# Kernel optimization log

Hardware: AMD Instinct MI355X
Metric: run time of the kernel (lower is better)

## Reference

```python
import jax, jax.numpy as jnp
import numpy as np

B, T, V, D, OUT = 32, 100, 10000, 128, 1000
CODE_P = 0.003  # ~30 active codes per visit


def gru_dir(x3, whh, bhh, reverse):
    """x3: [B,T,3F] precomputed input-side gates (W_ih x + b_ih). PyTorch GRU math."""
    F = whh.shape[1]
    h0 = jnp.zeros((x3.shape[0], F), x3.dtype)

    def step(h, xt):
        gh = h @ whh.T + bhh
        xr, xz, xn = jnp.split(xt, 3, -1)
        hr, hz, hn = jnp.split(gh, 3, -1)
        r = jax.nn.sigmoid(xr + hr)
        z = jax.nn.sigmoid(xz + hz)
        n = jnp.tanh(xn + r * hn)
        h_new = (1.0 - z) * n + z * h
        return h_new, h_new

    _, hs = jax.lax.scan(step, h0, jnp.swapaxes(x3, 0, 1), reverse=reverse)
    return jnp.swapaxes(hs, 0, 1)  # [B,T,F]


def setup_inputs() -> dict:
    key = jax.random.key(0)
    ks = jax.random.split(key, 16)
    s = lambda k, *sh: jax.random.normal(k, sh, dtype=jnp.float32) * 0.05
    # multi-hot visits, ~0/1 with density CODE_P; force code 0 present so no all-zero visit
    x = (jax.random.uniform(ks[0], (B, T, V)) < CODE_P).astype(jnp.float32)
    x = x.at[:, :, 0].set(1.0)
    return {
        "batchdata": x,
        "emb": s(ks[1], V, D),
        "wih_f": s(ks[2], 3 * D, D), "whh_f": s(ks[3], 3 * D, D),
        "bih_f": jnp.zeros((3 * D,), jnp.float32), "bhh_f": jnp.zeros((3 * D,), jnp.float32),
        "wih_b": s(ks[4], 3 * D, D), "whh_b": s(ks[5], 3 * D, D),
        "bih_b": jnp.zeros((3 * D,), jnp.float32), "bhh_b": jnp.zeros((3 * D,), jnp.float32),
        "attn_w": s(ks[6], 2 * D, 1), "attn_b": jnp.zeros((1,), jnp.float32),
        "comb_w": s(ks[7], D, 4 * D), "comb_b": jnp.zeros((D,), jnp.float32),
        "fc_w": s(ks[8], OUT, D), "fc_b": jnp.zeros((OUT,), jnp.float32),
    }


def reference(batchdata, emb, wih_f, whh_f, bih_f, bhh_f, wih_b, whh_b, bih_b, bhh_b,
              attn_w, attn_b, comb_w, comb_b, fc_w, fc_b):
    # multihot_to_embedding: sum of embedding rows where visit==1 == multihot @ table
    e = jnp.einsum('btv,vd->btd', batchdata, emb)          # [B,T,D]
    mask = jnp.any(e != 0, axis=2)                          # [B,T]
    # DipoleLayer: bidirectional GRU (hidden=D each dir), dropout in eval mode = identity
    xf = jnp.einsum('btf,gf->btg', e, wih_f) + bih_f
    xb = jnp.einsum('btf,gf->btg', e, wih_b) + bih_b
    hf = gru_dir(xf, whh_f, bhh_f, reverse=False)
    hb = gru_dir(xb, whh_b, bhh_b, reverse=True)
    h = jnp.concatenate([hf, hb], axis=-1)                  # [B,T,2D]
    # location-based attention over timesteps
    scores = (h @ attn_w)[..., 0] + attn_b[0]               # [B,T]
    scores = jnp.where(mask, scores, jnp.float32(-1e9))
    a = jax.nn.softmax(scores, axis=-1)
    c = jnp.einsum('bt,btf->bf', a, h)                      # [B,2D] context
    last = jnp.sum(mask.astype(jnp.int32), axis=-1) - 1     # last valid visit
    h_last = h[jnp.arange(h.shape[0]), last]                # [B,2D]
    feat = jnp.tanh(jnp.concatenate([c, h_last], -1) @ comb_w.T + comb_b)  # [B,D]
    logits = feat @ fc_w.T + fc_b                           # [B,OUT]
    return logits
```

## Files before the change

### kernel.cpp

```cpp
#include <hip/hip_runtime.h>
#include <math.h>

#define BB 32
#define TT 100
#define VV 10000
#define DD 128
#define OUTN 1000
#define G3 384

__global__ __launch_bounds__(256) void k_embed(
    const float* __restrict__ x, const float* __restrict__ emb,
    float* __restrict__ e, int* __restrict__ mask)
{
    const int bt  = blockIdx.x;
    const int tid = threadIdx.x;
    __shared__ int   s_cnt;
    __shared__ int   s_any;
    __shared__ int   s_idx[256];
    __shared__ float s_val[256];
    if (tid == 0) { s_cnt = 0; s_any = 0; }
    __syncthreads();

    const float4* x4 = (const float4*)(x + (size_t)bt * VV);
    for (int i = tid; i < VV / 4; i += 256) {
        float4 v = x4[i];
        if (v.x != 0.f) { int p = atomicAdd(&s_cnt, 1); if (p < 256) { s_idx[p] = 4*i+0; s_val[p] = v.x; } }
        if (v.y != 0.f) { int p = atomicAdd(&s_cnt, 1); if (p < 256) { s_idx[p] = 4*i+1; s_val[p] = v.y; } }
        if (v.z != 0.f) { int p = atomicAdd(&s_cnt, 1); if (p < 256) { s_idx[p] = 4*i+2; s_val[p] = v.z; } }
        if (v.w != 0.f) { int p = atomicAdd(&s_cnt, 1); if (p < 256) { s_idx[p] = 4*i+3; s_val[p] = v.w; } }
    }
    __syncthreads();
    int cnt = s_cnt; if (cnt > 256) cnt = 256;
    if (tid < DD) {
        float acc = 0.f;
        for (int i = 0; i < cnt; ++i)
            acc += s_val[i] * emb[(size_t)s_idx[i] * DD + tid];
        e[(size_t)bt * DD + tid] = acc;
        if (acc != 0.f) s_any = 1;
    }
    __syncthreads();
    if (tid == 0) mask[bt] = s_any;
}

__global__ __launch_bounds__(256) void k_gates(
    const float* __restrict__ e,
    const float* __restrict__ wih_f, const float* __restrict__ bih_f,
    const float* __restrict__ wih_b, const float* __restrict__ bih_b,
    float* __restrict__ x3)
{
    const int r0  = blockIdx.x * 8;
    const int tid = threadIdx.x;
    __shared__ __align__(16) float se[8][DD];
    for (int i = tid; i < 8 * DD; i += 256)
        se[i >> 7][i & 127] = e[(size_t)(r0 + (i >> 7)) * DD + (i & 127)];
    __syncthreads();

    for (int cc = 0; cc < 3; ++cc) {
        const int col = tid + cc * 256;
        const float* wrow;
        float bias;
        if (col < G3) { wrow = wih_f + (size_t)col * DD;        bias = bih_f[col]; }
        else          { wrow = wih_b + (size_t)(col - G3) * DD; bias = bih_b[col - G3]; }
        float acc[8];
        #pragma unroll
        for (int r = 0; r < 8; ++r) acc[r] = 0.f;
        const float4* w4 = (const float4*)wrow;
        for (int k4 = 0; k4 < DD / 4; ++k4) {
            float4 w = w4[k4];
            #pragma unroll
            for (int r = 0; r < 8; ++r) {
                float4 ev = *(const float4*)&se[r][4 * k4];
                acc[r] += ev.x * w.x + ev.y * w.y + ev.z * w.z + ev.w * w.w;
            }
        }
        #pragma unroll
        for (int r = 0; r < 8; ++r)
            x3[(size_t)(r0 + r) * 768 + col] = acc[r] + bias;
    }
}

__device__ __forceinline__ float4 ld_pin_b128(const float4* p)
{
    float4 r;
    asm volatile("global_load_dwordx4 %0, %1, off" : "=v"(r) : "v"(p));
    return r;
}

__global__ __launch_bounds__(512, 2) void k_gru(
    const float* __restrict__ x3,
    const float* __restrict__ whh_f, const float* __restrict__ bhh_f,
    const float* __restrict__ whh_b, const float* __restrict__ bhh_b,
    float* __restrict__ h_all)
{
    const int dir = blockIdx.x & 1;
    const int b   = blockIdx.x >> 1;
    const int tid = threadIdx.x;
    const int g   = tid & 127;
    const int kq  = tid >> 7;
    const int kb  = kq * 32;
    const float* whh = dir ? whh_b : whh_f;
    const float* bhh = dir ? bhh_b : bhh_f;

    const float4* pr4 = (const float4*)(whh + (size_t)(g         ) * DD + kb);
    const float4* pz4 = (const float4*)(whh + (size_t)(DD     + g) * DD + kb);
    const float4* pn4 = (const float4*)(whh + (size_t)(2 * DD + g) * DD + kb);

#define Q8(M) M(0) M(1) M(2) M(3) M(4) M(5) M(6) M(7)
#define DECLW(i) float4 wr##i = ld_pin_b128(pr4 + (i)); \
                 float4 wz##i = ld_pin_b128(pz4 + (i)); \
                 float4 wn##i = ld_pin_b128(pn4 + (i));
    Q8(DECLW)
#undef DECLW
    asm volatile("s_waitcnt vmcnt(0)" ::: "memory");
    __builtin_amdgcn_sched_barrier(0);

    float bhr = 0.f, bhz = 0.f, bhn = 0.f;
    if (tid < DD) { bhr = bhh[g]; bhz = bhh[DD + g]; bhn = bhh[2 * DD + g]; }

    __shared__ __align__(16) float h_lds[DD];
    __shared__ float p_lds[9 * DD];
    float h_reg = 0.f;
    if (tid < DD) h_lds[tid] = 0.f;

    float xr = 0.f, xz = 0.f, xn = 0.f;
    {
        const float* x3p = x3 + (size_t)(b * TT + (dir ? TT - 1 : 0)) * 768 + dir * G3;
        if (tid < DD) { xr = x3p[g]; xz = x3p[DD + g]; xn = x3p[2 * DD + g]; }
    }
    __syncthreads();

    for (int t = 0; t < TT; ++t) {
        const int te = dir ? (TT - 1 - t) : t;

        float nxr = 0.f, nxz = 0.f, nxn = 0.f;
        if (t + 1 < TT) {
            const int tn = dir ? (TT - 2 - t) : (t + 1);
            const float* x3n = x3 + (size_t)(b * TT + tn) * 768 + dir * G3;
            if (tid < DD) { nxr = x3n[g]; nxz = x3n[DD + g]; nxn = x3n[2 * DD + g]; }
        }

        float ar0 = 0.f, ar1 = 0.f, az0 = 0.f, az1 = 0.f, an0 = 0.f, an1 = 0.f;
#define FMA(i) { float4 hv = *(const float4*)&h_lds[kb + 4 * (i)]; \
        (((i)&1) ? ar1 : ar0) += wr##i.x*hv.x + wr##i.y*hv.y + wr##i.z*hv.z + wr##i.w*hv.w; \
        (((i)&1) ? az1 : az0) += wz##i.x*hv.x + wz##i.y*hv.y + wz##i.z*hv.z + wz##i.w*hv.w; \
        (((i)&1) ? an1 : an0) += wn##i.x*hv.x + wn##i.y*hv.y + wn##i.z*hv.z + wn##i.w*hv.w; }
        Q8(FMA)
#undef FMA
        const float pr = ar0 + ar1, pz = az0 + az1, pn = an0 + an1;

        if (kq) {
            const int q = (kq - 1) * 3;
            p_lds[(q + 0) * DD + g] = pr;
            p_lds[(q + 1) * DD + g] = pz;
            p_lds[(q + 2) * DD + g] = pn;
        }
        __syncthreads();

        if (tid < DD) {
            float hr = pr + p_lds[0*DD+g] + p_lds[3*DD+g] + p_lds[6*DD+g] + bhr;
            float hz = pz + p_lds[1*DD+g] + p_lds[4*DD+g] + p_lds[7*DD+g] + bhz;
            float hn = pn + p_lds[2*DD+g] + p_lds[5*DD+g] + p_lds[8*DD+g] + bhn;
            float r  = __builtin_amdgcn_rcpf(1.f + __expf(-(xr + hr)));
            float z  = __builtin_amdgcn_rcpf(1.f + __expf(-(xz + hz)));
            float e2 = __expf(2.f * (xn + r * hn));
            float n  = 1.f - 2.f * __builtin_amdgcn_rcpf(e2 + 1.f);
            float hnew = n + z * (h_reg - n);
            h_reg = hnew;
            h_lds[g] = hnew;
            h_all[(size_t)((dir * BB + b) * TT + te) * DD + g] = hnew;
        }
        __syncthreads();
        xr = nxr; xz = nxz; xn = nxn;
    }
#undef Q8
}

__global__ __launch_bounds__(256) void k_attn(
    const float* __restrict__ h_all, const int* __restrict__ mask,
    const float* __restrict__ attn_w, const float* __restrict__ attn_b,
    const float* __restrict__ comb_w, const float* __restrict__ comb_b,
    float* __restrict__ feat)
{
    const int b   = blockIdx.x;
    const int tid = threadIdx.x;
    __shared__ float s_aw[256];
    __shared__ float s_sc[128];
    __shared__ int   s_m[128];
    __shared__ float s_red[128];
    __shared__ __align__(16) float s_ch[512];

    s_aw[tid] = attn_w[tid];
    int m = 0;
    if (tid < 128) {
        m = (tid < TT) ? mask[b * TT + tid] : 0;
        s_m[tid] = m;
    }
    __syncthreads();
    for (int s = 64; s > 0; s >>= 1) {
        if (tid < s) s_m[tid] += s_m[tid + s];
        __syncthreads();
    }
    const int last = s_m[0] - 1;

    const float* hf = h_all + (size_t)(0 * BB + b) * TT * DD;
    const float* hb = h_all + (size_t)(1 * BB + b) * TT * DD;

    float sc = -1e9f;
    if (tid < TT) {
        float a = attn_b[0];
        const float4* hf4 = (const float4*)(hf + (size_t)tid * DD);
        const float4* hb4 = (const float4*)(hb + (size_t)tid * DD);
        for (int k = 0; k < DD / 4; ++k) {
            float4 v = hf4[k];
            a += v.x * s_aw[4*k] + v.y * s_aw[4*k+1] + v.z * s_aw[4*k+2] + v.w * s_aw[4*k+3];
        }
        for (int k = 0; k < DD / 4; ++k) {
            float4 v = hb4[k];
            a += v.x * s_aw[DD+4*k] + v.y * s_aw[DD+4*k+1] + v.z * s_aw[DD+4*k+2] + v.w * s_aw[DD+4*k+3];
        }
        sc = m ? a : -1e9f;
    }
    if (tid < 128) { s_sc[tid] = sc; s_red[tid] = sc; }
    __syncthreads();
    for (int s = 64; s > 0; s >>= 1) {
        if (tid < s) s_red[tid] = fmaxf(s_red[tid], s_red[tid + s]);
        __syncthreads();
    }
    const float mx = s_red[0];
    __syncthreads();
    float ex = 0.f;
    if (tid < 128) { ex = __expf(s_sc[tid] - mx); s_sc[tid] = ex; s_red[tid] = ex; }
    __syncthreads();
    for (int s = 64; s > 0; s >>= 1) {
        if (tid < s) s_red[tid] += s_red[tid + s];
        __syncthreads();
    }
    const float inv = 1.f / s_red[0];
    __syncthreads();

    {
        const int fl = tid & 127;
        const float* hp = (tid < 128) ? hf : hb;
        float csum = 0.f;
        for (int t = 0; t < TT; ++t)
            csum += s_sc[t] * hp[(size_t)t * DD + fl];
        s_ch[tid]       = csum * inv;
        s_ch[256 + tid] = hp[(size_t)last * DD + fl];
    }
    __syncthreads();

    if (tid < 128) {
        float a = comb_b[tid];
        const float4* cw = (const float4*)(comb_w + (size_t)tid * 512);
        for (int k = 0; k < 128; ++k) {
            float4 w4 = cw[k];
            float4 v4 = *(const float4*)&s_ch[4 * k];
            a += w4.x * v4.x + w4.y * v4.y + w4.z * v4.z + w4.w * v4.w;
        }
        feat[(size_t)b * DD + tid] = tanhf(a);
    }
}

__global__ __launch_bounds__(256) void k_logits(
    const float* __restrict__ feat, const float* __restrict__ fc_w,
    const float* __restrict__ fc_b, float* __restrict__ out)
{
    const int b   = blockIdx.x >> 2;
    const int oc  = blockIdx.x & 3;
    const int tid = threadIdx.x;
    const int o   = oc * 256 + tid;
    __shared__ __align__(16) float s_f[DD];
    if (tid < DD) s_f[tid] = feat[(size_t)b * DD + tid];
    __syncthreads();
    if (o < OUTN) {
        float a = fc_b[o];
        const float4* w4 = (const float4*)(fc_w + (size_t)o * DD);
        for (int k = 0; k < DD / 4; ++k) {
            float4 w = w4[k];
            float4 v = *(const float4*)&s_f[4 * k];
            a += w.x * v.x + w.y * v.y + w.z * v.z + w.w * v.w;
        }
        out[(size_t)b * OUTN + o] = a;
    }
}

extern "C" void kernel_launch(void* const* d_in, const int* in_sizes, int n_in,
                              void* d_out, int out_size, void* d_ws, size_t ws_size,
                              hipStream_t stream)
{
    const float* x      = (const float*)d_in[0];
    const float* emb    = (const float*)d_in[1];
    const float* wih_f  = (const float*)d_in[2];
    const float* whh_f  = (const float*)d_in[3];
    const float* bih_f  = (const float*)d_in[4];
    const float* bhh_f  = (const float*)d_in[5];
    const float* wih_b  = (const float*)d_in[6];
    const float* whh_b  = (const float*)d_in[7];
    const float* bih_b  = (const float*)d_in[8];
    const float* bhh_b  = (const float*)d_in[9];
    const float* attn_w = (const float*)d_in[10];
    const float* attn_b = (const float*)d_in[11];
    const float* comb_w = (const float*)d_in[12];
    const float* comb_b = (const float*)d_in[13];
    const float* fc_w   = (const float*)d_in[14];
    const float* fc_b   = (const float*)d_in[15];
    float* out = (float*)d_out;

    float* ws    = (float*)d_ws;
    float* e     = ws;
    int*   mask  = (int*)(ws + 409600);
    float* x3    = ws + 412800;
    float* h_all = ws + 2870400;
    float* feat  = ws + 3689600;

    k_embed <<<BB * TT,      256, 0, stream>>>(x, emb, e, mask);
    k_gates <<<(BB * TT)/8,  256, 0, stream>>>(e, wih_f, bih_f, wih_b, bih_b, x3);
    k_gru   <<<2 * BB,       512, 0, stream>>>(x3, whh_f, bhh_f, whh_b, bhh_b, h_all);
    k_attn  <<<BB,           256, 0, stream>>>(h_all, mask, attn_w, attn_b, comb_w, comb_b, feat);
    k_logits<<<BB * 4,       256, 0, stream>>>(feat, fc_w, fc_b, out);
}
```

Baseline: 354.5 us.

## Fuse embedding into gate GEMM and logits into attention kernel

The multi-hot embedding gather now happens inside the gate-projection kernel, so each block builds 8 embedding rows in shared memory and never writes or rereads the intermediate e buffer. The gather is unrolled into four independent accumulators. The final FC layer moves into the attention kernel, dropping one launch and the feat round-trip. The GRU launch bound changes from 2 to 1 blocks per SM, which frees registers. The trade-off is that the embed stage drops from 3200 blocks to 400, each scanning 8 rows serially, and the logits stage runs on only 32 blocks.

```diff
diff --git a/kernel.cpp b/kernel.cpp
--- a/kernel.cpp
+++ b/kernel.cpp
@@ -8,53 +8,51 @@
 #define OUTN 1000
 #define G3 384
 
-__global__ __launch_bounds__(256) void k_embed(
+__global__ __launch_bounds__(256) void k_embgate(
     const float* __restrict__ x, const float* __restrict__ emb,
-    float* __restrict__ e, int* __restrict__ mask)
-{
-    const int bt  = blockIdx.x;
+    const float* __restrict__ wih_f, const float* __restrict__ bih_f,
+    const float* __restrict__ wih_b, const float* __restrict__ bih_b,
+    float* __restrict__ x3, int* __restrict__ mask)
+{
+    const int r0  = blockIdx.x * 8;
     const int tid = threadIdx.x;
     __shared__ int   s_cnt;
     __shared__ int   s_any;
     __shared__ int   s_idx[256];
     __shared__ float s_val[256];
-    if (tid == 0) { s_cnt = 0; s_any = 0; }
-    __syncthreads();
-
-    const float4* x4 = (const float4*)(x + (size_t)bt * VV);
-    for (int i = tid; i < VV / 4; i += 256) {
-        float4 v = x4[i];
-        if (v.x != 0.f) { int p = atomicAdd(&s_cnt, 1); if (p < 256) { s_idx[p] = 4*i+0; s_val[p] = v.x; } }
-        if (v.y != 0.f) { int p = atomicAdd(&s_cnt, 1); if (p < 256) { s_idx[p] = 4*i+1; s_val[p] = v.y; } }
-        if (v.z != 0.f) { int p = atomicAdd(&s_cnt, 1); if (p < 256) { s_idx[p] = 4*i+2; s_val[p] = v.z; } }
-        if (v.w != 0.f) { int p = atomicAdd(&s_cnt, 1); if (p < 256) { s_idx[p] = 4*i+3; s_val[p] = v.w; } }
-    }
-    __syncthreads();
-    int cnt = s_cnt; if (cnt > 256) cnt = 256;
-    if (tid < DD) {
-        float acc = 0.f;
-        for (int i = 0; i < cnt; ++i)
-            acc += s_val[i] * emb[(size_t)s_idx[i] * DD + tid];
-        e[(size_t)bt * DD + tid] = acc;
-        if (acc != 0.f) s_any = 1;
-    }
-    __syncthreads();
-    if (tid == 0) mask[bt] = s_any;
-}
-
-__global__ __launch_bounds__(256) void k_gates(
-    const float* __restrict__ e,
-    const float* __restrict__ wih_f, const float* __restrict__ bih_f,
-    const float* __restrict__ wih_b, const float* __restrict__ bih_b,
-    float* __restrict__ x3)
-{
-    const int r0  = blockIdx.x * 8;
-    const int tid = threadIdx.x;
     __shared__ __align__(16) float se[8][DD];
-    for (int i = tid; i < 8 * DD; i += 256)
-        se[i >> 7][i & 127] = e[(size_t)(r0 + (i >> 7)) * DD + (i & 127)];
-    __syncthreads();
-
+
+    for (int r = 0; r < 8; ++r) {
+        if (tid == 0) { s_cnt = 0; s_any = 0; }
+        __syncthreads();
+        const float4* x4 = (const float4*)(x + (size_t)(r0 + r) * VV);
+        for (int i = tid; i < VV / 4; i += 256) {
+            float4 v = x4[i];
+            if (v.x != 0.f) { int p = atomicAdd(&s_cnt, 1); if (p < 256) { s_idx[p] = 4*i+0; s_val[p] = v.x; } }
+            if (v.y != 0.f) { int p = atomicAdd(&s_cnt, 1); if (p < 256) { s_idx[p] = 4*i+1; s_val[p] = v.y; } }
+            if (v.z != 0.f) { int p = atomicAdd(&s_cnt, 1); if (p < 256) { s_idx[p] = 4*i+2; s_val[p] = v.z; } }
+            if (v.w != 0.f) { int p = atomicAdd(&s_cnt, 1); if (p < 256) { s_idx[p] = 4*i+3; s_val[p] = v.w; } }
+        }
+        __syncthreads();
+        int cnt = s_cnt; if (cnt > 256) cnt = 256;
+        if (tid < DD) {
+            float a0 = 0.f, a1 = 0.f, a2 = 0.f, a3 = 0.f;
+            int i = 0;
+            for (; i + 3 < cnt; i += 4) {
+                a0 += s_val[i+0] * emb[(size_t)s_idx[i+0] * DD + tid];
+                a1 += s_val[i+1] * emb[(size_t)s_idx[i+1] * DD + tid];
+                a2 += s_val[i+2] * emb[(size_t)s_idx[i+2] * DD + tid];
+                a3 += s_val[i+3] * emb[(size_t)s_idx[i+3] * DD + tid];
+            }
+            for (; i < cnt; ++i)
+                a0 += s_val[i] * emb[(size_t)s_idx[i] * DD + tid];
+            float acc = (a0 + a1) + (a2 + a3);
+            se[r][tid] = acc;
+            if (acc != 0.f) s_any = 1;
+        }
+        __syncthreads();
+        if (tid == 0) mask[r0 + r] = s_any;
+    }
     for (int cc = 0; cc < 3; ++cc) {
         const int col = tid + cc * 256;
         const float* wrow;
@@ -86,7 +84,7 @@
     return r;
 }
 
-__global__ __launch_bounds__(512, 2) void k_gru(
+__global__ __launch_bounds__(512, 1) void k_gru(
     const float* __restrict__ x3,
     const float* __restrict__ whh_f, const float* __restrict__ bhh_f,
     const float* __restrict__ whh_b, const float* __restrict__ bhh_b,
@@ -175,11 +173,12 @@
 #undef Q8
 }
 
-__global__ __launch_bounds__(256) void k_attn(
+__global__ __launch_bounds__(256) void k_attn_logits(
     const float* __restrict__ h_all, const int* __restrict__ mask,
     const float* __restrict__ attn_w, const float* __restrict__ attn_b,
     const float* __restrict__ comb_w, const float* __restrict__ comb_b,
-    float* __restrict__ feat)
+    const float* __restrict__ fc_w, const float* __restrict__ fc_b,
+    float* __restrict__ out)
 {
     const int b   = blockIdx.x;
     const int tid = threadIdx.x;
@@ -188,6 +187,7 @@
     __shared__ int   s_m[128];
     __shared__ float s_red[128];
     __shared__ __align__(16) float s_ch[512];
+    __shared__ __align__(16) float s_feat[128];
 
     s_aw[tid] = attn_w[tid];
     int m = 0;
@@ -257,30 +257,23 @@
             float4 v4 = *(const float4*)&s_ch[4 * k];
             a += w4.x * v4.x + w4.y * v4.y + w4.z * v4.z + w4.w * v4.w;
         }
-        feat[(size_t)b * DD + tid] = tanhf(a);
-    }
-}
-
-__global__ __launch_bounds__(256) void k_logits(
-    const float* __restrict__ feat, const float* __restrict__ fc_w,
-    const float* __restrict__ fc_b, float* __restrict__ out)
-{
-    const int b   = blockIdx.x >> 2;
-    const int oc  = blockIdx.x & 3;
-    const int tid = threadIdx.x;
-    const int o   = oc * 256 + tid;
-    __shared__ __align__(16) float s_f[DD];
-    if (tid < DD) s_f[tid] = feat[(size_t)b * DD + tid];
-    __syncthreads();
-    if (o < OUTN) {
-        float a = fc_b[o];
-        const float4* w4 = (const float4*)(fc_w + (size_t)o * DD);
-        for (int k = 0; k < DD / 4; ++k) {
-            float4 w = w4[k];
-            float4 v = *(const float4*)&s_f[4 * k];
-            a += w.x * v.x + w.y * v.y + w.z * v.z + w.w * v.w;
-        }
-        out[(size_t)b * OUTN + o] = a;
+        s_feat[tid] = tanhf(a);
+    }
+    __syncthreads();
+
+    #pragma unroll
+    for (int j = 0; j < 4; ++j) {
+        const int o = j * 256 + tid;
+        if (o < OUTN) {
+            float a = fc_b[o];
+            const float4* w4 = (const float4*)(fc_w + (size_t)o * DD);
+            for (int k = 0; k < DD / 4; ++k) {
+                float4 w = w4[k];
+                float4 v = *(const float4*)&s_feat[4 * k];
+                a += w.x * v.x + w.y * v.y + w.z * v.z + w.w * v.w;
+            }
+            out[(size_t)b * OUTN + o] = a;
+        }
     }
 }
 
@@ -307,15 +300,11 @@
     float* out = (float*)d_out;
 
     float* ws    = (float*)d_ws;
-    float* e     = ws;
-    int*   mask  = (int*)(ws + 409600);
-    float* x3    = ws + 412800;
-    float* h_all = ws + 2870400;
-    float* feat  = ws + 3689600;
-
-    k_embed <<<BB * TT,      256, 0, stream>>>(x, emb, e, mask);
-    k_gates <<<(BB * TT)/8,  256, 0, stream>>>(e, wih_f, bih_f, wih_b, bih_b, x3);
-    k_gru   <<<2 * BB,       512, 0, stream>>>(x3, whh_f, bhh_f, whh_b, bhh_b, h_all);
-    k_attn  <<<BB,           256, 0, stream>>>(h_all, mask, attn_w, attn_b, comb_w, comb_b, feat);
-    k_logits<<<BB * 4,       256, 0, stream>>>(feat, fc_w, fc_b, out);
-}
+    float* x3    = ws;
+    float* h_all = ws + 2457600;
+    int*   mask  = (int*)(ws + 3276800);
+
+    k_embgate     <<<(BB * TT)/8, 256, 0, stream>>>(x, emb, wih_f, bih_f, wih_b, bih_b, x3, mask);
+    k_gru         <<<2 * BB,      512, 0, stream>>>(x3, whh_f, bhh_f, whh_b, bhh_b, h_all);
+    k_attn_logits <<<BB,          256, 0, stream>>>(h_all, mask, attn_w, attn_b, comb_w, comb_b, fc_w, fc_b, out);
+}
```

Result: slower. 407.4 us (+14.9%).
